# Kernel optimization log

Measured on AMD Instinct MI355X. Metric: run time of the kernel, lower is better.

The kernel has to match this reference:

```python
import jax, jax.numpy as jnp
import numpy as np

B, N, M, H = 16, 2048, 512, 512


def setup_inputs() -> dict:
    key = jax.random.key(0)
    ks = jax.random.split(key, 14)
    s = 0.02  # weight init scale
    return {
        "A": jax.random.uniform(ks[0], (B, N, N), dtype=jnp.float32),
        "h": jax.random.normal(ks[1], (B, N, M), dtype=jnp.float32),
        # fcv: Linear(m,H) -> ReLU -> Linear(H,H); weights stored [in,out]
        "Wv1": jax.random.normal(ks[2], (M, H), dtype=jnp.float32) * s,
        "bv1": jnp.zeros((H,), jnp.float32),
        "Wv2": jax.random.normal(ks[3], (H, H), dtype=jnp.float32) * s,
        "bv2": jnp.zeros((H,), jnp.float32),
        "Wk": jax.random.normal(ks[4], (M, H), dtype=jnp.float32) * s,
        "bk": jnp.zeros((H,), jnp.float32),
        "Wq": jax.random.normal(ks[5], (M, H), dtype=jnp.float32) * s,
        "bq": jnp.zeros((H,), jnp.float32),
        "Wout": jax.random.normal(ks[6], (H, M), dtype=jnp.float32) * s,
        "bout": jnp.zeros((M,), jnp.float32),
    }


def reference(A, h, Wv1, bv1, Wv2, bv2, Wk, bk, Wq, bq, Wout, bout):
    # v = relu(fcv(h)) where fcv = Lin -> ReLU -> Lin
    v = jax.nn.relu(jax.nn.relu(h @ Wv1 + bv1) @ Wv2 + bv2)      # [B,N,H]
    q = jax.nn.relu(h @ Wq + bq)                                  # [B,N,H]
    k = jax.nn.relu(h @ Wk + bk)                                  # [B,N,H]
    # att = softmax((q @ k^T) * -A, axis=2)
    scores = jnp.einsum("bnh,bmh->bnm", q, k) * -A                # [B,N,N]
    att = jax.nn.softmax(scores, axis=2)
    out = jnp.einsum("bnm,bmh->bnh", att, v) + v                  # [B,N,H]
    return jax.nn.relu(out @ Wout + bout)                         # [B,N,M]
```

## Files before the change

kernel.cpp:

```cpp
#include <hip/hip_runtime.h>

typedef __bf16 bf16;
typedef bf16 bf16x4 __attribute__((ext_vector_type(4)));
typedef bf16 bf16x8 __attribute__((ext_vector_type(8)));
typedef float f32x4 __attribute__((ext_vector_type(4)));

static constexpr int BATCH = 16;
static constexpr int SEQ   = 2048;
static constexpr int DH    = 512;
static constexpr int ROWS  = BATCH * SEQ;

__device__ __forceinline__ f32x4 mfma16(bf16x8 a, bf16x8 b, f32x4 c) {
    return __builtin_amdgcn_mfma_f32_16x16x32_bf16(a, b, c, 0, 0, 0);
}

__device__ __forceinline__ void gl_lds16(const bf16* g, bf16* l) {
    __builtin_amdgcn_global_load_lds((const __attribute__((address_space(1))) void*)g,
                                     (__attribute__((address_space(3))) void*)l, 16, 0, 0);
}

__global__ void cvt_bf16_kernel(const float* __restrict__ in, bf16* __restrict__ out, int n4) {
    int i = blockIdx.x * blockDim.x + threadIdx.x;
    const int stride = gridDim.x * blockDim.x;
    for (; i < n4; i += stride) {
        f32x4 f = *reinterpret_cast<const f32x4*>(in + (size_t)i * 4);
        bf16x4 o;
        o[0] = (bf16)f[0]; o[1] = (bf16)f[1]; o[2] = (bf16)f[2]; o[3] = (bf16)f[3];
        *reinterpret_cast<bf16x4*>(out + (size_t)i * 4) = o;
    }
}

__global__ void cvt_wT5_kernel(const float* __restrict__ w0, const float* __restrict__ w1,
                               const float* __restrict__ w2, const float* __restrict__ w3,
                               const float* __restrict__ w4, bf16* __restrict__ out) {
    const int t = blockIdx.y;
    const float* in = (t == 0) ? w0 : (t == 1) ? w1 : (t == 2) ? w2 : (t == 3) ? w3 : w4;
    int idx = blockIdx.x * 256 + threadIdx.x;
    int n = idx >> 9, k = idx & 511;
    out[t * 262144 + idx] = (bf16)in[k * 512 + n];
}

template <int OMODE>
__global__ __launch_bounds__(256, 2)
void gemm_relu_kernel(const bf16* __restrict__ X, const bf16* __restrict__ Wt,
                      const float* __restrict__ bias,
                      bf16* __restrict__ Y, bf16* __restrict__ Yt,
                      float* __restrict__ Yf)
{
    __shared__ bf16 Xl[2][128 * 64];
    __shared__ bf16 Wl[2][128 * 64];

    const int tid = threadIdx.x;
    const int lane = tid & 63, wid = tid >> 6;
    const int wr = wid >> 1, wc = wid & 1;
    const int r0 = blockIdx.x * 128;
    const int c0 = blockIdx.y * 128;
    const int lrow = lane & 15, lhi = lane >> 4;

    const int srow = tid >> 3;
    const int skb  = (tid & 7) ^ (srow & 7);
    const int sdst = wid * 512;

    auto stage = [&](int buf, int kc) {
        const bf16* xs = X + (size_t)r0 * 512 + kc * 64;
        const bf16* ws = Wt + (size_t)c0 * 512 + kc * 64;
        #pragma unroll
        for (int c = 0; c < 4; ++c) {
            const int row = c * 32 + srow;
            gl_lds16(xs + (size_t)row * 512 + skb * 8, &Xl[buf][c * 2048 + sdst]);
        }
        #pragma unroll
        for (int c = 0; c < 4; ++c) {
            const int row = c * 32 + srow;
            gl_lds16(ws + (size_t)row * 512 + skb * 8, &Wl[buf][c * 2048 + sdst]);
        }
    };

    f32x4 acc[4][4] = {};

    stage(0, 0);
    __syncthreads();

    for (int t = 0; t < 8; ++t) {
        const int buf = t & 1;
        if (t + 1 < 8) stage(buf ^ 1, t + 1);
        #pragma unroll
        for (int kk = 0; kk < 2; ++kk) {
            bf16x8 af[4], bfr[4];
            const int kb = kk * 4 + lhi;
            #pragma unroll
            for (int tt = 0; tt < 4; ++tt) {
                const int ra = wr * 64 + tt * 16 + lrow;
                af[tt] = *reinterpret_cast<const bf16x8*>(&Xl[buf][ra * 64 + ((kb ^ (ra & 7)) * 8)]);
            }
            #pragma unroll
            for (int tt = 0; tt < 4; ++tt) {
                const int rb = wc * 64 + tt * 16 + lrow;
                bfr[tt] = *reinterpret_cast<const bf16x8*>(&Wl[buf][rb * 64 + ((kb ^ (rb & 7)) * 8)]);
            }
            #pragma unroll
            for (int i = 0; i < 4; ++i)
                #pragma unroll
                for (int j = 0; j < 4; ++j)
                    acc[i][j] = mfma16(af[i], bfr[j], acc[i][j]);
        }
        __syncthreads();
    }

    #pragma unroll
    for (int i = 0; i < 4; ++i) {
        #pragma unroll
        for (int j = 0; j < 4; ++j) {
            const int col = c0 + wc * 64 + j * 16 + lrow;
            const float bb = bias[col];
            #pragma unroll
            for (int rg = 0; rg < 4; ++rg) {
                const int r = r0 + wr * 64 + i * 16 + lhi * 4 + rg;
                float y = acc[i][j][rg] + bb;
                y = y > 0.f ? y : 0.f;
                if (OMODE == 2) {
                    Yf[(size_t)r * 512 + col] = y;
                } else {
                    Y[(size_t)r * 512 + col] = (bf16)y;
                    if (OMODE == 1) {
                        const int bi = r >> 11, nn = r & 2047;
                        Yt[((size_t)bi * 512 + col) * 2048 + nn] = (bf16)y;
                    }
                }
            }
        }
    }
}

__global__ __launch_bounds__(512, 1)
void attn_kernel(const bf16* __restrict__ Q, const bf16* __restrict__ K,
                 const bf16* __restrict__ Vt, const bf16* __restrict__ V,
                 const float* __restrict__ A, bf16* __restrict__ O)
{
    __shared__ bf16 K_lds[2][64 * 512];
    __shared__ bf16 P_lds[64 * 72];
    __shared__ float sump_lds[2][64];

    const int tid = threadIdx.x;
    const int lane = tid & 63, wid = tid >> 6;
    const int wr = wid >> 1, wc = wid & 1;
    const int lrow = lane & 15, lhi = lane >> 4;

    const int id = blockIdx.x;
    const int xcd = id & 7, j = id >> 3;
    const int bb = 2 * xcd + (j >> 5);
    const int n0 = (j & 31) * 64;
    const int srow_base = wr * 16 + lhi * 4;

    const bf16* Kbase  = K + (size_t)bb * SEQ * DH;
    const bf16* Vtbase = Vt + (size_t)bb * DH * SEQ;

    #pragma unroll
    for (int c = 0; c < 8; ++c) {
        const int row = wid * 8 + c;
        gl_lds16(Kbase + (size_t)row * DH + ((lane ^ (row & 7)) * 8), &K_lds[0][row * 512]);
    }

    bf16x8 qf[16];
    {
        const bf16* qp = Q + (size_t)(bb * SEQ + n0 + wr * 16 + lrow) * DH + lhi * 8;
        #pragma unroll
        for (int kk = 0; kk < 16; ++kk)
            qf[kk] = *reinterpret_cast<const bf16x8*>(qp + kk * 32);
    }

    float av_c[8];
    {
        const float* ap = A + ((size_t)bb * SEQ + n0 + srow_base) * SEQ + wc * 32 + lrow;
        #pragma unroll
        for (int rg = 0; rg < 4; ++rg) {
            av_c[rg]     = ap[(size_t)rg * SEQ];
            av_c[rg + 4] = ap[(size_t)rg * SEQ + 16];
        }
    }

    float l_part[4] = {};
    f32x4 acc[4][4] = {};

    __syncthreads();

    for (int it = 0; it < 32; ++it) {
        const int m0 = it * 64;
        const int buf = it & 1;

        if (it + 1 < 32) {
            #pragma unroll
            for (int c = 0; c < 8; ++c) {
                const int row = wid * 8 + c;
                gl_lds16(Kbase + (size_t)(m0 + 64 + row) * DH + ((lane ^ (row & 7)) * 8),
                         &K_lds[buf ^ 1][row * 512]);
            }
        }
        bf16x8 vf[4][2];
        {
            const bf16* vp = Vtbase + (size_t)(wid * 64 + lrow) * SEQ + m0 + lhi * 8;
            #pragma unroll
            for (int ht = 0; ht < 4; ++ht)
                #pragma unroll
                for (int kc = 0; kc < 2; ++kc)
                    vf[ht][kc] = *reinterpret_cast<const bf16x8*>(
                        vp + (size_t)(ht * 16) * SEQ + kc * 32);
        }
        float av_n[8];
        if (it + 1 < 32) {
            const float* ap = A + ((size_t)bb * SEQ + n0 + srow_base) * SEQ + m0 + 64 + wc * 32 + lrow;
            #pragma unroll
            for (int rg = 0; rg < 4; ++rg) {
                av_n[rg]     = ap[(size_t)rg * SEQ];
                av_n[rg + 4] = ap[(size_t)rg * SEQ + 16];
            }
        }

        f32x4 s0 = {}, s1 = {};
        {
            const int kr0 = wc * 32 + lrow, kr1 = kr0 + 16;
            #pragma unroll
            for (int kk = 0; kk < 16; ++kk) {
                const int ks = kk * 4 + lhi;
                bf16x8 k0 = *reinterpret_cast<const bf16x8*>(
                    &K_lds[buf][kr0 * 512 + ((ks ^ (kr0 & 7)) * 8)]);
                bf16x8 k1 = *reinterpret_cast<const bf16x8*>(
                    &K_lds[buf][kr1 * 512 + ((ks ^ (kr1 & 7)) * 8)]);
                s0 = mfma16(qf[kk], k0, s0);
                s1 = mfma16(qf[kk], k1, s1);
            }
        }

        #pragma unroll
        for (int rg = 0; rg < 4; ++rg) {
            const float p0 = __expf(s0[rg] * (-av_c[rg]));
            const float p1 = __expf(s1[rg] * (-av_c[rg + 4]));
            const int row = srow_base + rg;
            const int c0i = wc * 32 + lrow;
            P_lds[row * 72 + c0i]      = (bf16)p0;
            P_lds[row * 72 + c0i + 16] = (bf16)p1;
            l_part[rg] += p0 + p1;
        }

        asm volatile("s_waitcnt lgkmcnt(0)" ::: "memory");
        __builtin_amdgcn_s_barrier();
        __builtin_amdgcn_sched_barrier(0);

        #pragma unroll
        for (int t = 0; t < 4; ++t) {
            bf16x8 pf[2];
            #pragma unroll
            for (int kc = 0; kc < 2; ++kc)
                pf[kc] = *reinterpret_cast<const bf16x8*>(
                    &P_lds[(t * 16 + lrow) * 72 + kc * 32 + lhi * 8]);
            #pragma unroll
            for (int ht = 0; ht < 4; ++ht)
                #pragma unroll
                for (int kc = 0; kc < 2; ++kc)
                    acc[t][ht] = mfma16(pf[kc], vf[ht][kc], acc[t][ht]);
        }

        asm volatile("s_waitcnt lgkmcnt(0)" ::: "memory");
        __builtin_amdgcn_s_barrier();
        __builtin_amdgcn_sched_barrier(0);

        #pragma unroll
        for (int q = 0; q < 8; ++q) av_c[q] = av_n[q];
    }

    #pragma unroll
    for (int rg = 0; rg < 4; ++rg) {
        float s = l_part[rg];
        s += __shfl_xor(s, 1);
        s += __shfl_xor(s, 2);
        s += __shfl_xor(s, 4);
        s += __shfl_xor(s, 8);
        if (lrow == 0) sump_lds[wc][srow_base + rg] = s;
    }
    __syncthreads();

    #pragma unroll
    for (int t = 0; t < 4; ++t) {
        #pragma unroll
        for (int rg = 0; rg < 4; ++rg) {
            const int row = t * 16 + lhi * 4 + rg;
            const float inv = 1.f / (sump_lds[0][row] + sump_lds[1][row]);
            const size_t rbase = (size_t)(bb * SEQ + n0 + row) * DH;
            #pragma unroll
            for (int ht = 0; ht < 4; ++ht) {
                const int col = wid * 64 + ht * 16 + lrow;
                const float vv = (float)V[rbase + col];
                O[rbase + col] = (bf16)(acc[t][ht][rg] * inv + vv);
            }
        }
    }
}

extern "C" void kernel_launch(void* const* d_in, const int* in_sizes, int n_in,
                              void* d_out, int out_size, void* d_ws, size_t ws_size,
                              hipStream_t stream) {
    const float* A    = (const float*)d_in[0];
    const float* h    = (const float*)d_in[1];
    const float* Wv1  = (const float*)d_in[2];
    const float* bv1  = (const float*)d_in[3];
    const float* Wv2  = (const float*)d_in[4];
    const float* bv2  = (const float*)d_in[5];
    const float* Wk   = (const float*)d_in[6];
    const float* bk   = (const float*)d_in[7];
    const float* Wq   = (const float*)d_in[8];
    const float* bq   = (const float*)d_in[9];
    const float* Wout = (const float*)d_in[10];
    const float* bout = (const float*)d_in[11];
    float* out = (float*)d_out;

    char* ws = (char*)d_ws;
    const size_t SZ = (size_t)ROWS * 512 * sizeof(bf16);
    bf16* hb   = (bf16*)(ws + 0 * SZ);
    bf16* tq   = (bf16*)(ws + 1 * SZ);
    bf16* kb   = (bf16*)(ws + 2 * SZ);
    bf16* vb   = (bf16*)(ws + 3 * SZ);
    bf16* vtb  = (bf16*)(ws + 4 * SZ);
    bf16* wbase = (bf16*)(ws + 5 * SZ);
    bf16* Wv1t  = wbase + 0 * 262144;
    bf16* Wv2t  = wbase + 1 * 262144;
    bf16* Wqt   = wbase + 2 * 262144;
    bf16* Wkt   = wbase + 3 * 262144;
    bf16* Woutt = wbase + 4 * 262144;
    bf16* ob = hb;

    cvt_bf16_kernel<<<4096, 256, 0, stream>>>(h, hb, ROWS * 512 / 4);
    cvt_wT5_kernel<<<dim3(1024, 5), 256, 0, stream>>>(Wv1, Wv2, Wq, Wk, Wout, wbase);

    dim3 gg(ROWS / 128, 512 / 128);
    gemm_relu_kernel<0><<<gg, 256, 0, stream>>>(hb, Wv1t, bv1, tq, nullptr, nullptr);
    gemm_relu_kernel<1><<<gg, 256, 0, stream>>>(tq, Wv2t, bv2, vb, vtb, nullptr);
    gemm_relu_kernel<0><<<gg, 256, 0, stream>>>(hb, Wqt, bq, tq, nullptr, nullptr);
    gemm_relu_kernel<0><<<gg, 256, 0, stream>>>(hb, Wkt, bk, kb, nullptr, nullptr);

    attn_kernel<<<dim3(512), 512, 0, stream>>>(tq, kb, vtb, vb, A, ob);

    gemm_relu_kernel<2><<<gg, 256, 0, stream>>>(ob, Woutt, bout, nullptr, nullptr, out);
}
```

Baseline: 505.2 us.

## Widen attention key tile to 128 and drop K double buffering

The attention loop now processes 128 keys per iteration with a single 128-row K buffer in LDS instead of a double-buffered 64-row one. The next K tile is loaded after the score barrier, so it overlaps the P·V phase rather than the score phase. The A prefetch into registers is removed and A is loaded at the start of each iteration. V fragments are loaded in a two-stage register ring inside the PV loop. This halves the barrier count and loop overhead per key, at the cost of exposed A load latency and K load latency that is no longer hidden behind a whole score phase.

```diff
diff --git a/kernel.cpp b/kernel.cpp
--- a/kernel.cpp
+++ b/kernel.cpp
@@ -137,8 +137,8 @@
                  const bf16* __restrict__ Vt, const bf16* __restrict__ V,
                  const float* __restrict__ A, bf16* __restrict__ O)
 {
-    __shared__ bf16 K_lds[2][64 * 512];
-    __shared__ bf16 P_lds[64 * 72];
+    __shared__ bf16 K_lds[128 * 512];
+    __shared__ bf16 P_lds[64 * 144];
     __shared__ float sump_lds[2][64];
 
     const int tid = threadIdx.x;
@@ -156,9 +156,9 @@
     const bf16* Vtbase = Vt + (size_t)bb * DH * SEQ;
 
     #pragma unroll
-    for (int c = 0; c < 8; ++c) {
-        const int row = wid * 8 + c;
-        gl_lds16(Kbase + (size_t)row * DH + ((lane ^ (row & 7)) * 8), &K_lds[0][row * 512]);
+    for (int c = 0; c < 16; ++c) {
+        const int row = wid * 16 + c;
+        gl_lds16(Kbase + (size_t)row * DH + ((lane ^ (row & 7)) * 8), &K_lds[row * 512]);
     }
 
     bf16x8 qf[16];
@@ -169,113 +169,101 @@
             qf[kk] = *reinterpret_cast<const bf16x8*>(qp + kk * 32);
     }
 
-    float av_c[8];
-    {
-        const float* ap = A + ((size_t)bb * SEQ + n0 + srow_base) * SEQ + wc * 32 + lrow;
-        #pragma unroll
-        for (int rg = 0; rg < 4; ++rg) {
-            av_c[rg]     = ap[(size_t)rg * SEQ];
-            av_c[rg + 4] = ap[(size_t)rg * SEQ + 16];
-        }
-    }
-
     float l_part[4] = {};
     f32x4 acc[4][4] = {};
 
     __syncthreads();
 
-    for (int it = 0; it < 32; ++it) {
-        const int m0 = it * 64;
-        const int buf = it & 1;
-
-        if (it + 1 < 32) {
-            #pragma unroll
-            for (int c = 0; c < 8; ++c) {
-                const int row = wid * 8 + c;
-                gl_lds16(Kbase + (size_t)(m0 + 64 + row) * DH + ((lane ^ (row & 7)) * 8),
-                         &K_lds[buf ^ 1][row * 512]);
-            }
-        }
-        bf16x8 vf[4][2];
+    for (int it = 0; it < 16; ++it) {
+        const int m0 = it * 128;
+
+        float av[16];
         {
-            const bf16* vp = Vtbase + (size_t)(wid * 64 + lrow) * SEQ + m0 + lhi * 8;
-            #pragma unroll
-            for (int ht = 0; ht < 4; ++ht)
+            const float* ap = A + ((size_t)bb * SEQ + n0 + srow_base) * SEQ + m0 + wc * 64 + lrow;
+            #pragma unroll
+            for (int sc = 0; sc < 4; ++sc)
                 #pragma unroll
-                for (int kc = 0; kc < 2; ++kc)
-                    vf[ht][kc] = *reinterpret_cast<const bf16x8*>(
-                        vp + (size_t)(ht * 16) * SEQ + kc * 32);
-        }
-        float av_n[8];
-        if (it + 1 < 32) {
-            const float* ap = A + ((size_t)bb * SEQ + n0 + srow_base) * SEQ + m0 + 64 + wc * 32 + lrow;
-            #pragma unroll
-            for (int rg = 0; rg < 4; ++rg) {
-                av_n[rg]     = ap[(size_t)rg * SEQ];
-                av_n[rg + 4] = ap[(size_t)rg * SEQ + 16];
-            }
-        }
-
-        f32x4 s0 = {}, s1 = {};
+                for (int rg = 0; rg < 4; ++rg)
+                    av[sc * 4 + rg] = ap[(size_t)rg * SEQ + sc * 16];
+        }
+
+        f32x4 s[4] = {};
         {
-            const int kr0 = wc * 32 + lrow, kr1 = kr0 + 16;
             #pragma unroll
             for (int kk = 0; kk < 16; ++kk) {
                 const int ks = kk * 4 + lhi;
-                bf16x8 k0 = *reinterpret_cast<const bf16x8*>(
-                    &K_lds[buf][kr0 * 512 + ((ks ^ (kr0 & 7)) * 8)]);
-                bf16x8 k1 = *reinterpret_cast<const bf16x8*>(
-                    &K_lds[buf][kr1 * 512 + ((ks ^ (kr1 & 7)) * 8)]);
-                s0 = mfma16(qf[kk], k0, s0);
-                s1 = mfma16(qf[kk], k1, s1);
-            }
-        }
-
-        #pragma unroll
-        for (int rg = 0; rg < 4; ++rg) {
-            const float p0 = __expf(s0[rg] * (-av_c[rg]));
-            const float p1 = __expf(s1[rg] * (-av_c[rg + 4]));
-            const int row = srow_base + rg;
-            const int c0i = wc * 32 + lrow;
-            P_lds[row * 72 + c0i]      = (bf16)p0;
-            P_lds[row * 72 + c0i + 16] = (bf16)p1;
-            l_part[rg] += p0 + p1;
+                #pragma unroll
+                for (int sc = 0; sc < 4; ++sc) {
+                    const int kr = wc * 64 + sc * 16 + lrow;
+                    bf16x8 kf = *reinterpret_cast<const bf16x8*>(
+                        &K_lds[kr * 512 + ((ks ^ (kr & 7)) * 8)]);
+                    s[sc] = mfma16(qf[kk], kf, s[sc]);
+                }
+            }
+        }
+
+        #pragma unroll
+        for (int sc = 0; sc < 4; ++sc) {
+            #pragma unroll
+            for (int rg = 0; rg < 4; ++rg) {
+                const float p = __expf(s[sc][rg] * (-av[sc * 4 + rg]));
+                const int row = srow_base + rg;
+                P_lds[row * 144 + wc * 64 + sc * 16 + lrow] = (bf16)p;
+                l_part[rg] += p;
+            }
         }
 
         asm volatile("s_waitcnt lgkmcnt(0)" ::: "memory");
         __builtin_amdgcn_s_barrier();
         __builtin_amdgcn_sched_barrier(0);
 
-        #pragma unroll
-        for (int t = 0; t < 4; ++t) {
-            bf16x8 pf[2];
-            #pragma unroll
-            for (int kc = 0; kc < 2; ++kc)
-                pf[kc] = *reinterpret_cast<const bf16x8*>(
-                    &P_lds[(t * 16 + lrow) * 72 + kc * 32 + lhi * 8]);
+        if (it + 1 < 16) {
+            #pragma unroll
+            for (int c = 0; c < 16; ++c) {
+                const int row = wid * 16 + c;
+                gl_lds16(Kbase + (size_t)(m0 + 128 + row) * DH + ((lane ^ (row & 7)) * 8),
+                         &K_lds[row * 512]);
+            }
+        }
+
+        {
+            const bf16* vp = Vtbase + (size_t)(wid * 64 + lrow) * SEQ + m0 + lhi * 8;
+            bf16x8 vfk[2][4];
             #pragma unroll
             for (int ht = 0; ht < 4; ++ht)
+                vfk[0][ht] = *reinterpret_cast<const bf16x8*>(vp + (size_t)(ht * 16) * SEQ);
+            #pragma unroll
+            for (int kc = 0; kc < 4; ++kc) {
+                if (kc + 1 < 4) {
+                    #pragma unroll
+                    for (int ht = 0; ht < 4; ++ht)
+                        vfk[(kc + 1) & 1][ht] = *reinterpret_cast<const bf16x8*>(
+                            vp + (size_t)(ht * 16) * SEQ + (kc + 1) * 32);
+                }
                 #pragma unroll
-                for (int kc = 0; kc < 2; ++kc)
-                    acc[t][ht] = mfma16(pf[kc], vf[ht][kc], acc[t][ht]);
+                for (int t = 0; t < 4; ++t) {
+                    const bf16x8 pf = *reinterpret_cast<const bf16x8*>(
+                        &P_lds[(t * 16 + lrow) * 144 + kc * 32 + lhi * 8]);
+                    #pragma unroll
+                    for (int ht = 0; ht < 4; ++ht)
+                        acc[t][ht] = mfma16(pf, vfk[kc & 1][ht], acc[t][ht]);
+                }
+            }
         }
 
         asm volatile("s_waitcnt lgkmcnt(0)" ::: "memory");
         __builtin_amdgcn_s_barrier();
         __builtin_amdgcn_sched_barrier(0);
-
-        #pragma unroll
-        for (int q = 0; q < 8; ++q) av_c[q] = av_n[q];
     }
 
     #pragma unroll
     for (int rg = 0; rg < 4; ++rg) {
-        float s = l_part[rg];
-        s += __shfl_xor(s, 1);
-        s += __shfl_xor(s, 2);
-        s += __shfl_xor(s, 4);
-        s += __shfl_xor(s, 8);
-        if (lrow == 0) sump_lds[wc][srow_base + rg] = s;
+        float sv = l_part[rg];
+        sv += __shfl_xor(sv, 1);
+        sv += __shfl_xor(sv, 2);
+        sv += __shfl_xor(sv, 4);
+        sv += __shfl_xor(sv, 8);
+        if (lrow == 0) sump_lds[wc][srow_base + rg] = sv;
     }
     __syncthreads();
 
```

New measurement: 500.7 us. About the same (-0.9%).

## Stage A tiles through LDS and single-buffer K loaded during PV phase

Applied to the files above, without the earlier changes.

The attention loop now loads the A scaling tile with asynchronous global-to-LDS copies into a double buffer, instead of per-thread register loads. The K tile drops from two LDS buffers to one. The next K tile is issued after the softmax barrier, so it overlaps only the P·V phase. V fragment loads move after that barrier as well. This aims to cut register pressure and scattered A loads, but K and V load latency now has less compute to hide behind, because they are no longer prefetched a full iteration ahead.

```diff
diff --git a/kernel.cpp b/kernel.cpp
--- a/kernel.cpp
+++ b/kernel.cpp
@@ -14,7 +14,7 @@
     return __builtin_amdgcn_mfma_f32_16x16x32_bf16(a, b, c, 0, 0, 0);
 }
 
-__device__ __forceinline__ void gl_lds16(const bf16* g, bf16* l) {
+__device__ __forceinline__ void gl_lds16(const void* g, void* l) {
     __builtin_amdgcn_global_load_lds((const __attribute__((address_space(1))) void*)g,
                                      (__attribute__((address_space(3))) void*)l, 16, 0, 0);
 }
@@ -137,7 +137,8 @@
                  const bf16* __restrict__ Vt, const bf16* __restrict__ V,
                  const float* __restrict__ A, bf16* __restrict__ O)
 {
-    __shared__ bf16 K_lds[2][64 * 512];
+    __shared__ bf16 K_lds[64 * 512];
+    __shared__ float A_lds[2][64 * 64];
     __shared__ bf16 P_lds[64 * 72];
     __shared__ float sump_lds[2][64];
 
@@ -154,12 +155,23 @@
 
     const bf16* Kbase  = K + (size_t)bb * SEQ * DH;
     const bf16* Vtbase = Vt + (size_t)bb * DH * SEQ;
+    const float* Abase = A + ((size_t)bb * SEQ + n0) * SEQ;
+
+    auto stageA = [&](int ab, int m0n) {
+        #pragma unroll
+        for (int c = 0; c < 2; ++c) {
+            const int row = wid * 8 + c * 4 + (lane >> 4);
+            gl_lds16(Abase + (size_t)row * SEQ + m0n + (lane & 15) * 4,
+                     &A_lds[ab][(wid * 8 + c * 4) * 64]);
+        }
+    };
 
     #pragma unroll
     for (int c = 0; c < 8; ++c) {
         const int row = wid * 8 + c;
-        gl_lds16(Kbase + (size_t)row * DH + ((lane ^ (row & 7)) * 8), &K_lds[0][row * 512]);
-    }
+        gl_lds16(Kbase + (size_t)row * DH + ((lane ^ (row & 7)) * 8), &K_lds[row * 512]);
+    }
+    stageA(0, 0);
 
     bf16x8 qf[16];
     {
@@ -169,113 +181,97 @@
             qf[kk] = *reinterpret_cast<const bf16x8*>(qp + kk * 32);
     }
 
-    float av_c[8];
-    {
-        const float* ap = A + ((size_t)bb * SEQ + n0 + srow_base) * SEQ + wc * 32 + lrow;
-        #pragma unroll
-        for (int rg = 0; rg < 4; ++rg) {
-            av_c[rg]     = ap[(size_t)rg * SEQ];
-            av_c[rg + 4] = ap[(size_t)rg * SEQ + 16];
-        }
-    }
-
     float l_part[4] = {};
     f32x4 acc[4][4] = {};
 
     __syncthreads();
 
+    int abuf = 0;
     for (int it = 0; it < 32; ++it) {
         const int m0 = it * 64;
-        const int buf = it & 1;
+
+        if (it + 1 < 32) stageA(abuf ^ 1, m0 + 64);
+
+        f32x4 s0 = {}, s1 = {};
+        {
+            const int kr0 = wc * 32 + lrow, kr1 = kr0 + 16;
+            #pragma unroll
+            for (int kk = 0; kk < 16; ++kk) {
+                const int ks = kk * 4 + lhi;
+                bf16x8 k0 = *reinterpret_cast<const bf16x8*>(
+                    &K_lds[kr0 * 512 + ((ks ^ (kr0 & 7)) * 8)]);
+                bf16x8 k1 = *reinterpret_cast<const bf16x8*>(
+                    &K_lds[kr1 * 512 + ((ks ^ (kr1 & 7)) * 8)]);
+                s0 = mfma16(qf[kk], k0, s0);
+                s1 = mfma16(qf[kk], k1, s1);
+            }
+        }
+
+        #pragma unroll
+        for (int rg = 0; rg < 4; ++rg) {
+            const int row = srow_base + rg;
+            const float a0 = A_lds[abuf][row * 64 + wc * 32 + lrow];
+            const float a1 = A_lds[abuf][row * 64 + wc * 32 + 16 + lrow];
+            const float p0 = __expf(s0[rg] * (-a0));
+            const float p1 = __expf(s1[rg] * (-a1));
+            const int c0i = wc * 32 + lrow;
+            P_lds[row * 72 + c0i]      = (bf16)p0;
+            P_lds[row * 72 + c0i + 16] = (bf16)p1;
+            l_part[rg] += p0 + p1;
+        }
+
+        asm volatile("s_waitcnt lgkmcnt(0)" ::: "memory");
+        __builtin_amdgcn_s_barrier();
+        __builtin_amdgcn_sched_barrier(0);
 
         if (it + 1 < 32) {
             #pragma unroll
             for (int c = 0; c < 8; ++c) {
                 const int row = wid * 8 + c;
                 gl_lds16(Kbase + (size_t)(m0 + 64 + row) * DH + ((lane ^ (row & 7)) * 8),
-                         &K_lds[buf ^ 1][row * 512]);
-            }
-        }
-        bf16x8 vf[4][2];
+                         &K_lds[row * 512]);
+            }
+        }
+
         {
             const bf16* vp = Vtbase + (size_t)(wid * 64 + lrow) * SEQ + m0 + lhi * 8;
+            bf16x8 vf[4][2];
             #pragma unroll
             for (int ht = 0; ht < 4; ++ht)
                 #pragma unroll
                 for (int kc = 0; kc < 2; ++kc)
                     vf[ht][kc] = *reinterpret_cast<const bf16x8*>(
                         vp + (size_t)(ht * 16) * SEQ + kc * 32);
-        }
-        float av_n[8];
-        if (it + 1 < 32) {
-            const float* ap = A + ((size_t)bb * SEQ + n0 + srow_base) * SEQ + m0 + 64 + wc * 32 + lrow;
-            #pragma unroll
-            for (int rg = 0; rg < 4; ++rg) {
-                av_n[rg]     = ap[(size_t)rg * SEQ];
-                av_n[rg + 4] = ap[(size_t)rg * SEQ + 16];
-            }
-        }
-
-        f32x4 s0 = {}, s1 = {};
-        {
-            const int kr0 = wc * 32 + lrow, kr1 = kr0 + 16;
-            #pragma unroll
-            for (int kk = 0; kk < 16; ++kk) {
-                const int ks = kk * 4 + lhi;
-                bf16x8 k0 = *reinterpret_cast<const bf16x8*>(
-                    &K_lds[buf][kr0 * 512 + ((ks ^ (kr0 & 7)) * 8)]);
-                bf16x8 k1 = *reinterpret_cast<const bf16x8*>(
-                    &K_lds[buf][kr1 * 512 + ((ks ^ (kr1 & 7)) * 8)]);
-                s0 = mfma16(qf[kk], k0, s0);
-                s1 = mfma16(qf[kk], k1, s1);
-            }
-        }
-
-        #pragma unroll
-        for (int rg = 0; rg < 4; ++rg) {
-            const float p0 = __expf(s0[rg] * (-av_c[rg]));
-            const float p1 = __expf(s1[rg] * (-av_c[rg + 4]));
-            const int row = srow_base + rg;
-            const int c0i = wc * 32 + lrow;
-            P_lds[row * 72 + c0i]      = (bf16)p0;
-            P_lds[row * 72 + c0i + 16] = (bf16)p1;
-            l_part[rg] += p0 + p1;
+            #pragma unroll
+            for (int t = 0; t < 4; ++t) {
+                bf16x8 pf[2];
+                #pragma unroll
+                for (int kc = 0; kc < 2; ++kc)
+                    pf[kc] = *reinterpret_cast<const bf16x8*>(
+                        &P_lds[(t * 16 + lrow) * 72 + kc * 32 + lhi * 8]);
+                #pragma unroll
+                for (int ht = 0; ht < 4; ++ht)
+                    #pragma unroll
+                    for (int kc = 0; kc < 2; ++kc)
+                        acc[t][ht] = mfma16(pf[kc], vf[ht][kc], acc[t][ht]);
+            }
         }
 
         asm volatile("s_waitcnt lgkmcnt(0)" ::: "memory");
         __builtin_amdgcn_s_barrier();
         __builtin_amdgcn_sched_barrier(0);
 
-        #pragma unroll
-        for (int t = 0; t < 4; ++t) {
-            bf16x8 pf[2];
-            #pragma unroll
-            for (int kc = 0; kc < 2; ++kc)
-                pf[kc] = *reinterpret_cast<const bf16x8*>(
-                    &P_lds[(t * 16 + lrow) * 72 + kc * 32 + lhi * 8]);
-            #pragma unroll
-            for (int ht = 0; ht < 4; ++ht)
-                #pragma unroll
-                for (int kc = 0; kc < 2; ++kc)
-                    acc[t][ht] = mfma16(pf[kc], vf[ht][kc], acc[t][ht]);
-        }
-
-        asm volatile("s_waitcnt lgkmcnt(0)" ::: "memory");
-        __builtin_amdgcn_s_barrier();
-        __builtin_amdgcn_sched_barrier(0);
-
-        #pragma unroll
-        for (int q = 0; q < 8; ++q) av_c[q] = av_n[q];
+        abuf ^= 1;
     }
 
     #pragma unroll
     for (int rg = 0; rg < 4; ++rg) {
-        float s = l_part[rg];
-        s += __shfl_xor(s, 1);
-        s += __shfl_xor(s, 2);
-        s += __shfl_xor(s, 4);
-        s += __shfl_xor(s, 8);
-        if (lrow == 0) sump_lds[wc][srow_base + rg] = s;
+        float sv = l_part[rg];
+        sv += __shfl_xor(sv, 1);
+        sv += __shfl_xor(sv, 2);
+        sv += __shfl_xor(sv, 4);
+        sv += __shfl_xor(sv, 8);
+        if (lrow == 0) sump_lds[wc][srow_base + rg] = sv;
     }
     __syncthreads();
 
```

Measured after the change: 524.3 us. 3.8% more time.

## Reshape attention warp tiling to 2x4 and target two waves per EU

Applied to the files above, without the earlier changes.

Changes the QK^T warp layout from 4x2 (16 rows x 32 cols per wave) to 2x4 (32 rows x 16 cols per wave), so each K fragment read from LDS feeds two MFMAs. The V fragment loads move from before the QK step to after the barrier, and the A values are no longer prefetched one iteration ahead; both changes cut live registers. Launch attributes now request two waves per EU so more waves can hide latency. The cost is that A and V global-load latency is no longer overlapped with the QK MFMAs, and the doubled Q fragments add registers.

```diff
diff --git a/kernel.cpp b/kernel.cpp
--- a/kernel.cpp
+++ b/kernel.cpp
@@ -14,7 +14,7 @@
     return __builtin_amdgcn_mfma_f32_16x16x32_bf16(a, b, c, 0, 0, 0);
 }
 
-__device__ __forceinline__ void gl_lds16(const bf16* g, bf16* l) {
+__device__ __forceinline__ void gl_lds16(const void* g, void* l) {
     __builtin_amdgcn_global_load_lds((const __attribute__((address_space(1))) void*)g,
                                      (__attribute__((address_space(3))) void*)l, 16, 0, 0);
 }
@@ -132,28 +132,28 @@
     }
 }
 
-__global__ __launch_bounds__(512, 1)
+__global__ __attribute__((amdgpu_flat_work_group_size(512, 512), amdgpu_waves_per_eu(2, 2)))
 void attn_kernel(const bf16* __restrict__ Q, const bf16* __restrict__ K,
                  const bf16* __restrict__ Vt, const bf16* __restrict__ V,
                  const float* __restrict__ A, bf16* __restrict__ O)
 {
     __shared__ bf16 K_lds[2][64 * 512];
     __shared__ bf16 P_lds[64 * 72];
-    __shared__ float sump_lds[2][64];
+    __shared__ float sump_lds[4][64];
 
     const int tid = threadIdx.x;
     const int lane = tid & 63, wid = tid >> 6;
-    const int wr = wid >> 1, wc = wid & 1;
+    const int wr = wid >> 2, wc = wid & 3;
     const int lrow = lane & 15, lhi = lane >> 4;
 
     const int id = blockIdx.x;
     const int xcd = id & 7, j = id >> 3;
     const int bb = 2 * xcd + (j >> 5);
     const int n0 = (j & 31) * 64;
-    const int srow_base = wr * 16 + lhi * 4;
 
     const bf16* Kbase  = K + (size_t)bb * SEQ * DH;
     const bf16* Vtbase = Vt + (size_t)bb * DH * SEQ;
+    const float* Abase = A + ((size_t)bb * SEQ + n0 + wr * 32 + lhi * 4) * SEQ + wc * 16 + lrow;
 
     #pragma unroll
     for (int c = 0; c < 8; ++c) {
@@ -161,25 +161,18 @@
         gl_lds16(Kbase + (size_t)row * DH + ((lane ^ (row & 7)) * 8), &K_lds[0][row * 512]);
     }
 
-    bf16x8 qf[16];
+    bf16x8 qf[2][16];
     {
-        const bf16* qp = Q + (size_t)(bb * SEQ + n0 + wr * 16 + lrow) * DH + lhi * 8;
-        #pragma unroll
-        for (int kk = 0; kk < 16; ++kk)
-            qf[kk] = *reinterpret_cast<const bf16x8*>(qp + kk * 32);
-    }
-
-    float av_c[8];
-    {
-        const float* ap = A + ((size_t)bb * SEQ + n0 + srow_base) * SEQ + wc * 32 + lrow;
-        #pragma unroll
-        for (int rg = 0; rg < 4; ++rg) {
-            av_c[rg]     = ap[(size_t)rg * SEQ];
-            av_c[rg + 4] = ap[(size_t)rg * SEQ + 16];
-        }
-    }
-
-    float l_part[4] = {};
+        const bf16* qp = Q + (size_t)(bb * SEQ + n0 + wr * 32 + lrow) * DH + lhi * 8;
+        #pragma unroll
+        for (int t2 = 0; t2 < 2; ++t2)
+            #pragma unroll
+            for (int kk = 0; kk < 16; ++kk)
+                qf[t2][kk] = *reinterpret_cast<const bf16x8*>(
+                    qp + (size_t)t2 * 16 * DH + kk * 32);
+    }
+
+    float l_part[2][4] = {};
     f32x4 acc[4][4] = {};
 
     __syncthreads();
@@ -196,86 +189,80 @@
                          &K_lds[buf ^ 1][row * 512]);
             }
         }
-        bf16x8 vf[4][2];
+        float av[8];
         {
-            const bf16* vp = Vtbase + (size_t)(wid * 64 + lrow) * SEQ + m0 + lhi * 8;
-            #pragma unroll
-            for (int ht = 0; ht < 4; ++ht)
+            const float* ap = Abase + m0;
+            #pragma unroll
+            for (int t2 = 0; t2 < 2; ++t2)
                 #pragma unroll
-                for (int kc = 0; kc < 2; ++kc)
-                    vf[ht][kc] = *reinterpret_cast<const bf16x8*>(
-                        vp + (size_t)(ht * 16) * SEQ + kc * 32);
-        }
-        float av_n[8];
-        if (it + 1 < 32) {
-            const float* ap = A + ((size_t)bb * SEQ + n0 + srow_base) * SEQ + m0 + 64 + wc * 32 + lrow;
-            #pragma unroll
-            for (int rg = 0; rg < 4; ++rg) {
-                av_n[rg]     = ap[(size_t)rg * SEQ];
-                av_n[rg + 4] = ap[(size_t)rg * SEQ + 16];
-            }
-        }
-
-        f32x4 s0 = {}, s1 = {};
+                for (int rg = 0; rg < 4; ++rg)
+                    av[t2 * 4 + rg] = ap[(size_t)(t2 * 16 + rg) * SEQ];
+        }
+
+        f32x4 s[2] = {};
         {
-            const int kr0 = wc * 32 + lrow, kr1 = kr0 + 16;
+            const int kr = wc * 16 + lrow;
             #pragma unroll
             for (int kk = 0; kk < 16; ++kk) {
                 const int ks = kk * 4 + lhi;
-                bf16x8 k0 = *reinterpret_cast<const bf16x8*>(
-                    &K_lds[buf][kr0 * 512 + ((ks ^ (kr0 & 7)) * 8)]);
-                bf16x8 k1 = *reinterpret_cast<const bf16x8*>(
-                    &K_lds[buf][kr1 * 512 + ((ks ^ (kr1 & 7)) * 8)]);
-                s0 = mfma16(qf[kk], k0, s0);
-                s1 = mfma16(qf[kk], k1, s1);
-            }
-        }
-
-        #pragma unroll
-        for (int rg = 0; rg < 4; ++rg) {
-            const float p0 = __expf(s0[rg] * (-av_c[rg]));
-            const float p1 = __expf(s1[rg] * (-av_c[rg + 4]));
-            const int row = srow_base + rg;
-            const int c0i = wc * 32 + lrow;
-            P_lds[row * 72 + c0i]      = (bf16)p0;
-            P_lds[row * 72 + c0i + 16] = (bf16)p1;
-            l_part[rg] += p0 + p1;
+                bf16x8 kf = *reinterpret_cast<const bf16x8*>(
+                    &K_lds[buf][kr * 512 + ((ks ^ (kr & 7)) * 8)]);
+                s[0] = mfma16(qf[0][kk], kf, s[0]);
+                s[1] = mfma16(qf[1][kk], kf, s[1]);
+            }
+        }
+
+        #pragma unroll
+        for (int t2 = 0; t2 < 2; ++t2) {
+            #pragma unroll
+            for (int rg = 0; rg < 4; ++rg) {
+                const float p = __expf(s[t2][rg] * (-av[t2 * 4 + rg]));
+                const int row = wr * 32 + t2 * 16 + lhi * 4 + rg;
+                P_lds[row * 72 + wc * 16 + lrow] = (bf16)p;
+                l_part[t2][rg] += p;
+            }
         }
 
         asm volatile("s_waitcnt lgkmcnt(0)" ::: "memory");
         __builtin_amdgcn_s_barrier();
         __builtin_amdgcn_sched_barrier(0);
 
-        #pragma unroll
-        for (int t = 0; t < 4; ++t) {
-            bf16x8 pf[2];
-            #pragma unroll
-            for (int kc = 0; kc < 2; ++kc)
-                pf[kc] = *reinterpret_cast<const bf16x8*>(
-                    &P_lds[(t * 16 + lrow) * 72 + kc * 32 + lhi * 8]);
-            #pragma unroll
-            for (int ht = 0; ht < 4; ++ht)
+        {
+            const bf16* vp = Vtbase + (size_t)(wid * 64 + lrow) * SEQ + m0 + lhi * 8;
+            #pragma unroll
+            for (int kc = 0; kc < 2; ++kc) {
+                bf16x8 vf[4];
                 #pragma unroll
-                for (int kc = 0; kc < 2; ++kc)
-                    acc[t][ht] = mfma16(pf[kc], vf[ht][kc], acc[t][ht]);
+                for (int ht = 0; ht < 4; ++ht)
+                    vf[ht] = *reinterpret_cast<const bf16x8*>(
+                        vp + (size_t)(ht * 16) * SEQ + kc * 32);
+                #pragma unroll
+                for (int t = 0; t < 4; ++t) {
+                    const bf16x8 pf = *reinterpret_cast<const bf16x8*>(
+                        &P_lds[(t * 16 + lrow) * 72 + kc * 32 + lhi * 8]);
+                    #pragma unroll
+                    for (int ht = 0; ht < 4; ++ht)
+                        acc[t][ht] = mfma16(pf, vf[ht], acc[t][ht]);
+                }
+            }
         }
 
         asm volatile("s_waitcnt lgkmcnt(0)" ::: "memory");
         __builtin_amdgcn_s_barrier();
         __builtin_amdgcn_sched_barrier(0);
-
-        #pragma unroll
-        for (int q = 0; q < 8; ++q) av_c[q] = av_n[q];
     }
 
     #pragma unroll
-    for (int rg = 0; rg < 4; ++rg) {
-        float s = l_part[rg];
-        s += __shfl_xor(s, 1);
-        s += __shfl_xor(s, 2);
-        s += __shfl_xor(s, 4);
-        s += __shfl_xor(s, 8);
-        if (lrow == 0) sump_lds[wc][srow_base + rg] = s;
+    for (int t2 = 0; t2 < 2; ++t2) {
+        #pragma unroll
+        for (int rg = 0; rg < 4; ++rg) {
+            float sv = l_part[t2][rg];
+            sv += __shfl_xor(sv, 1);
+            sv += __shfl_xor(sv, 2);
+            sv += __shfl_xor(sv, 4);
+            sv += __shfl_xor(sv, 8);
+            if (lrow == 0) sump_lds[wc][wr * 32 + t2 * 16 + lhi * 4 + rg] = sv;
+        }
     }
     __syncthreads();
 
@@ -284,7 +271,9 @@
         #pragma unroll
         for (int rg = 0; rg < 4; ++rg) {
             const int row = t * 16 + lhi * 4 + rg;
-            const float inv = 1.f / (sump_lds[0][row] + sump_lds[1][row]);
+            const float l = sump_lds[0][row] + sump_lds[1][row]
+                          + sump_lds[2][row] + sump_lds[3][row];
+            const float inv = 1.f / l;
             const size_t rbase = (size_t)(bb * SEQ + n0 + row) * DH;
             #pragma unroll
             for (int ht = 0; ht < 4; ++ht) {
```

After: 623.4 us. 23.4% more time.
